# Optimization experiments

Measured on AMD Instinct MI355X. Metric: run time of the kernel, lower is better.

Reference implementation:

```python
import jax, jax.numpy as jnp
import numpy as np

TOP_K = 10
RANKING_WEIGHT = 0.3
UP_WEIGHT = 1.0
DOWN_WEIGHT = 0.5
NEG = 1e9  # finite stand-in for -inf so softmax/grads stay NaN-free


def setup_inputs() -> dict:
    key = jax.random.key(0)
    k1, k2, k3, k4 = jax.random.split(key, 4)
    B, N = 1024, 5000
    up_logits = jax.random.normal(k1, (B, N), jnp.float32)
    down_logits = jax.random.normal(k2, (B, N), jnp.float32)
    y_true = jax.random.normal(k3, (B, N), jnp.float32) * 0.05  # daily returns
    masks = jax.random.randint(k4, (B, N), 0, 2).astype(jnp.int32)
    return {"up_logits": up_logits, "down_logits": down_logits,
            "y_true": y_true, "masks": masks}


def _bce_with_logits(x, z):
    # softplus(x) - x*z  ==  -[z*log(sig(x)) + (1-z)*log(1-sig(x))]
    return jax.nn.softplus(x) - x * z


def reference(up_logits, down_logits, y_true, masks):
    maskb = masks > 0                                   # [B, N]
    maskf = maskb.astype(up_logits.dtype)
    num_valid = maskf.sum(-1)                           # [B]
    nv_safe = jnp.maximum(num_valid, 1.0)
    k = jnp.minimum(TOP_K, num_valid.astype(jnp.int32))  # [B] min(top_k, num)

    # Descending rank of y_true among valid entries (invalid pushed to bottom).
    y_desc = jnp.where(maskb, y_true, -NEG)
    rank_desc = jnp.argsort(jnp.argsort(-y_desc, axis=-1), axis=-1)  # [B, N]
    up_labels = (rank_desc < k[:, None]).astype(up_logits.dtype)

    # Ascending rank (biggest losers) for down path.
    y_asc = jnp.where(maskb, y_true, NEG)
    rank_asc = jnp.argsort(jnp.argsort(y_asc, axis=-1), axis=-1)
    down_labels = (rank_asc < k[:, None]).astype(down_logits.dtype)

    # Mean BCE over valid entries per row.
    up_loss = jnp.sum(_bce_with_logits(up_logits, up_labels) * maskf, -1) / nv_safe
    down_loss = jnp.sum(_bce_with_logits(down_logits, down_labels) * maskf, -1) / nv_safe

    # Listwise KL: softmax over valid entries; kl_div(log p, q, 'batchmean')
    # with 1D input of size num divides the sum by num.
    logp = jax.nn.log_softmax(jnp.where(maskb, up_logits, -NEG), axis=-1)
    logq = jax.nn.log_softmax(jnp.where(maskb, y_true, -NEG), axis=-1)
    q = jnp.exp(logq)
    kl = jnp.sum(jnp.where(maskb, q * (logq - logp), 0.0), -1) / nv_safe

    batch_loss = UP_WEIGHT * up_loss + DOWN_WEIGHT * down_loss + RANKING_WEIGHT * kl
    batch_loss = jnp.where(num_valid > 0, batch_loss, 0.0)  # skip empty rows
    return jnp.sum(batch_loss) / up_logits.shape[0]
```

## Files before the change

### kernel.cpp

```cpp
#include <hip/hip_runtime.h>
#include <math.h>

#define NCOLS 5000
#define NF4   1250
#define BLOCK 256
#define NWAVES (BLOCK / 64)
#define NITER 5
#define TOPKK 10
#define CAP 128

__device__ __forceinline__ unsigned mono_f32(float f) {
  unsigned u = __float_as_uint(f);
  return (u & 0x80000000u) ? ~u : (u | 0x80000000u);
}

__device__ __forceinline__ float wave_sum_f(float v) {
#pragma unroll
  for (int o = 1; o < 64; o <<= 1) v += __shfl_xor(v, o);
  return v;
}
__device__ __forceinline__ int wave_sum_i(int v) {
#pragma unroll
  for (int o = 1; o < 64; o <<= 1) v += __shfl_xor(v, o);
  return v;
}
__device__ __forceinline__ unsigned wave_max_u(unsigned v) {
#pragma unroll
  for (int o = 1; o < 64; o <<= 1) {
    unsigned w = __shfl_xor(v, o);
    v = w > v ? w : v;
  }
  return v;
}

extern "C" __global__ __launch_bounds__(BLOCK, 4)
void row_loss_kernel(const float* __restrict__ up, const float* __restrict__ down,
                     const float* __restrict__ yt, const int* __restrict__ masks,
                     float* __restrict__ out, float inv_nrows) {
  __shared__ float red_f[6][NWAVES];
  __shared__ int red_i[NWAVES];
  __shared__ unsigned t1w_t[NWAVES];
  __shared__ unsigned t1w_b[NWAVES];
  __shared__ unsigned keys_t[CAP];
  __shared__ int      col_t[CAP];
  __shared__ unsigned keys_b[CAP];
  __shared__ int      col_b[CAP];
  __shared__ int ct, cb;
  __shared__ float s_res[2];

  const int tid = threadIdx.x;
  const int lane = tid & 63;
  const int wv = tid >> 6;
  const int row = blockIdx.x;
  const long long b4 = (long long)row * NF4;
  const long long base = (long long)row * NCOLS;

  const float4* up4 = (const float4*)up + b4;
  const float4* dn4 = (const float4*)down + b4;
  const float4* yt4 = (const float4*)yt + b4;
  const int4*   mk4 = (const int4*)masks + b4;

  if (tid == 0) { ct = 0; cb = 0; }

  float4 y4[NITER], u4[NITER], d4[NITER];
  int4 m4[NITER];
#pragma unroll
  for (int j = 0; j < NITER; ++j) {
    const int f = j * BLOCK + tid;
    const int fc = f < NF4 ? f : NF4 - 1;
    y4[j] = yt4[fc];
    u4[j] = up4[fc];
    d4[j] = dn4[fc];
    m4[j] = mk4[fc];
  }

  unsigned km[NITER][4];
  int nv_l = 0;
  float sq = 0.f, sp = 0.f, seyy = 0.f, seyu = 0.f, aspu = 0.f, aspd = 0.f;
  unsigned tmax = 0u, tbmax = 0u;
#pragma unroll
  for (int j = 0; j < NITER; ++j) {
    const bool inb = (j * BLOCK + tid) < NF4;
    const float* yp = (const float*)&y4[j];
    const float* upp = (const float*)&u4[j];
    const float* dp = (const float*)&d4[j];
    const int* mp = (const int*)&m4[j];
#pragma unroll
    for (int c = 0; c < 4; ++c) {
      const bool valid = inb && (mp[c] > 0);
      const float y = yp[c], u = upp[c], d = dp[c];
      const unsigned kd = valid ? mono_f32(y) : 0u;
      const unsigned kb = valid ? ~kd : 0u;
      km[j][c] = kd;
      tmax = kd > tmax ? kd : tmax;
      tbmax = kb > tbmax ? kb : tbmax;
      if (valid) {
        nv_l++;
        const float ey = __expf(y);
        sq += ey;
        seyy += ey * y;
        seyu += ey * u;
        sp += __expf(u);
        aspu += fmaxf(u, 0.f) + __logf(1.f + __expf(-fabsf(u)));
        aspd += fmaxf(d, 0.f) + __logf(1.f + __expf(-fabsf(d)));
      }
    }
  }

  nv_l = wave_sum_i(nv_l);
  sq = wave_sum_f(sq);
  sp = wave_sum_f(sp);
  seyy = wave_sum_f(seyy);
  seyu = wave_sum_f(seyu);
  aspu = wave_sum_f(aspu);
  aspd = wave_sum_f(aspd);
  if (lane == 0) {
    red_i[wv] = nv_l;
    red_f[0][wv] = sq;  red_f[1][wv] = sp;
    red_f[2][wv] = seyy; red_f[3][wv] = seyu;
    red_f[4][wv] = aspu; red_f[5][wv] = aspd;
  }

  {
    unsigned v = tmax, t1 = 0u;
#pragma unroll 1
    for (int r = 0; r < TOPKK; ++r) {
      unsigned m = wave_max_u(v);
      if (v == m) v = 0u;
      t1 = m;
    }
    if (lane == 0) t1w_t[wv] = t1;
  }
  {
    unsigned v = tbmax, t1 = 0u;
#pragma unroll 1
    for (int r = 0; r < TOPKK; ++r) {
      unsigned m = wave_max_u(v);
      if (v == m) v = 0u;
      t1 = m;
    }
    if (lane == 0) t1w_b[wv] = t1;
  }
  __syncthreads();

  int nv = 0;
#pragma unroll
  for (int w = 0; w < NWAVES; ++w) nv += red_i[w];
  const int k = nv < TOPKK ? nv : TOPKK;

  unsigned t1 = 0u, t1b = 0u;
#pragma unroll
  for (int w = 0; w < NWAVES; ++w) {
    t1 = t1w_t[w] > t1 ? t1w_t[w] : t1;
    t1b = t1w_b[w] > t1b ? t1w_b[w] : t1b;
  }

#pragma unroll
  for (int j = 0; j < NITER; ++j) {
#pragma unroll
    for (int c = 0; c < 4; ++c) {
      const unsigned kd = km[j][c];
      if (kd != 0u) {
        const int col = ((j * BLOCK + tid) << 2) + c;
        if (kd >= t1) {
          int i = atomicAdd(&ct, 1);
          if (i < CAP) { keys_t[i] = kd; col_t[i] = col; }
        }
        const unsigned kb = ~kd;
        if (kb >= t1b) {
          int i = atomicAdd(&cb, 1);
          if (i < CAP) { keys_b[i] = kb; col_b[i] = col; }
        }
      }
    }
  }
  __syncthreads();

  if (wv == 0) {
    const int n = ct < CAP ? ct : CAP;
    unsigned k0 = (lane < n) ? keys_t[lane] : 0u;
    unsigned k1 = (64 + lane < n) ? keys_t[64 + lane] : 0u;
    unsigned w0 = k0, w1 = k1;
    unsigned thr = 0xFFFFFFFFu;
#pragma unroll 1
    for (int r = 0; r < k; ++r) {
      unsigned m = wave_max_u(w0 > w1 ? w0 : w1);
      if (w0 == m) w0 = 0u;
      else if (w1 == m) w1 = 0u;
      thr = m;
    }
    float su = 0.f;
    if (k0 >= thr && k0 != 0u) su += up[base + col_t[lane]];
    if (k1 >= thr && k1 != 0u) su += up[base + col_t[64 + lane]];
    su = wave_sum_f(su);
    if (lane == 0) s_res[0] = su;
  } else if (wv == 1) {
    const int n = cb < CAP ? cb : CAP;
    unsigned k0 = (lane < n) ? keys_b[lane] : 0u;
    unsigned k1 = (64 + lane < n) ? keys_b[64 + lane] : 0u;
    unsigned w0 = k0, w1 = k1;
    unsigned thr = 0xFFFFFFFFu;
#pragma unroll 1
    for (int r = 0; r < k; ++r) {
      unsigned m = wave_max_u(w0 > w1 ? w0 : w1);
      if (w0 == m) w0 = 0u;
      else if (w1 == m) w1 = 0u;
      thr = m;
    }
    float sd = 0.f;
    if (k0 >= thr && k0 != 0u) sd += down[base + col_b[lane]];
    if (k1 >= thr && k1 != 0u) sd += down[base + col_b[64 + lane]];
    sd = wave_sum_f(sd);
    if (lane == 0) s_res[1] = sd;
  }
  __syncthreads();

  if (tid == 0 && nv > 0) {
    float SQ = 0.f, SP = 0.f, SYY = 0.f, SYU = 0.f, ASU = 0.f, ASD = 0.f;
#pragma unroll
    for (int w = 0; w < NWAVES; ++w) {
      SQ += red_f[0][w]; SP += red_f[1][w];
      SYY += red_f[2][w]; SYU += red_f[3][w];
      ASU += red_f[4][w]; ASD += red_f[5][w];
    }
    const float SU = s_res[0];
    const float SD = s_res[1];
    const float kl = (SYY - SYU) / SQ - __logf(SQ) + __logf(SP);
    const float up_loss = ASU - SU;
    const float dn_loss = ASD - SD;
    const float loss = (up_loss + 0.5f * dn_loss + 0.3f * kl) / (float)nv;
    atomicAdd(out, loss * inv_nrows);
  }
}

extern "C" void kernel_launch(void* const* d_in, const int* in_sizes, int n_in,
                              void* d_out, int out_size, void* d_ws, size_t ws_size,
                              hipStream_t stream) {
  const float* up_logits   = (const float*)d_in[0];
  const float* down_logits = (const float*)d_in[1];
  const float* y_true      = (const float*)d_in[2];
  const int*   masks       = (const int*)d_in[3];

  const int nrows = in_sizes[0] / NCOLS;

  hipMemsetAsync(d_out, 0, sizeof(float) * (size_t)out_size, stream);
  row_loss_kernel<<<nrows, BLOCK, 0, stream>>>(up_logits, down_logits, y_true,
                                               masks, (float*)d_out,
                                               1.0f / (float)nrows);
}
```

Before: 124.2 us.

## Use 1024-thread blocks per row with per-thread top-2 candidate tracking

Each row is now processed by 1024 threads instead of 256. Loads and math are fused into a single pass that reads two float4 slots per thread. To keep candidate sets tight with more waves, each thread keeps its top two keys instead of only its max, and the candidate buffers grow to 512 entries with an 8-way per-lane selection loop. Softplus is simplified to log(1+exp(x)), which reuses exp(u); this risks overflow for very large logits. Occupancy bounds change as well, which may constrain registers.

```diff
diff --git a/kernel.cpp b/kernel.cpp
--- a/kernel.cpp
+++ b/kernel.cpp
@@ -3,11 +3,11 @@
 
 #define NCOLS 5000
 #define NF4   1250
-#define BLOCK 256
+#define BLOCK 1024
 #define NWAVES (BLOCK / 64)
-#define NITER 5
+#define NITER 2
 #define TOPKK 10
-#define CAP 128
+#define CAP 512
 
 __device__ __forceinline__ unsigned mono_f32(float f) {
   unsigned u = __float_as_uint(f);
@@ -33,7 +33,7 @@
   return v;
 }
 
-extern "C" __global__ __launch_bounds__(BLOCK, 4)
+extern "C" __global__ __launch_bounds__(BLOCK, 8)
 void row_loss_kernel(const float* __restrict__ up, const float* __restrict__ down,
                      const float* __restrict__ yt, const int* __restrict__ masks,
                      float* __restrict__ out, float inv_nrows) {
@@ -62,29 +62,23 @@
 
   if (tid == 0) { ct = 0; cb = 0; }
 
-  float4 y4[NITER], u4[NITER], d4[NITER];
-  int4 m4[NITER];
+  unsigned km[NITER][4];
+  int nv_l = 0;
+  float sq = 0.f, sp = 0.f, seyy = 0.f, seyu = 0.f, aspu = 0.f, aspd = 0.f;
+  unsigned a0 = 0u, a1 = 0u, bb0 = 0u, bb1 = 0u;
 #pragma unroll
   for (int j = 0; j < NITER; ++j) {
     const int f = j * BLOCK + tid;
     const int fc = f < NF4 ? f : NF4 - 1;
-    y4[j] = yt4[fc];
-    u4[j] = up4[fc];
-    d4[j] = dn4[fc];
-    m4[j] = mk4[fc];
-  }
-
-  unsigned km[NITER][4];
-  int nv_l = 0;
-  float sq = 0.f, sp = 0.f, seyy = 0.f, seyu = 0.f, aspu = 0.f, aspd = 0.f;
-  unsigned tmax = 0u, tbmax = 0u;
-#pragma unroll
-  for (int j = 0; j < NITER; ++j) {
-    const bool inb = (j * BLOCK + tid) < NF4;
-    const float* yp = (const float*)&y4[j];
-    const float* upp = (const float*)&u4[j];
-    const float* dp = (const float*)&d4[j];
-    const int* mp = (const int*)&m4[j];
+    const float4 y4 = yt4[fc];
+    const float4 u4 = up4[fc];
+    const float4 d4 = dn4[fc];
+    const int4   m4 = mk4[fc];
+    const bool inb = f < NF4;
+    const float* yp = (const float*)&y4;
+    const float* upp = (const float*)&u4;
+    const float* dp = (const float*)&d4;
+    const int* mp = (const int*)&m4;
 #pragma unroll
     for (int c = 0; c < 4; ++c) {
       const bool valid = inb && (mp[c] > 0);
@@ -92,17 +86,19 @@
       const unsigned kd = valid ? mono_f32(y) : 0u;
       const unsigned kb = valid ? ~kd : 0u;
       km[j][c] = kd;
-      tmax = kd > tmax ? kd : tmax;
-      tbmax = kb > tbmax ? kb : tbmax;
+      if (kd > a1) { if (kd > a0) { a1 = a0; a0 = kd; } else a1 = kd; }
+      if (kb > bb1) { if (kb > bb0) { bb1 = bb0; bb0 = kb; } else bb1 = kb; }
       if (valid) {
         nv_l++;
         const float ey = __expf(y);
+        const float eu = __expf(u);
+        const float ed = __expf(d);
         sq += ey;
         seyy += ey * y;
         seyu += ey * u;
-        sp += __expf(u);
-        aspu += fmaxf(u, 0.f) + __logf(1.f + __expf(-fabsf(u)));
-        aspd += fmaxf(d, 0.f) + __logf(1.f + __expf(-fabsf(d)));
+        sp += eu;
+        aspu += __logf(1.f + eu);
+        aspd += __logf(1.f + ed);
       }
     }
   }
@@ -122,21 +118,23 @@
   }
 
   {
-    unsigned v = tmax, t1 = 0u;
+    unsigned v0 = a0, v1 = a1, t1 = 0u;
 #pragma unroll 1
     for (int r = 0; r < TOPKK; ++r) {
-      unsigned m = wave_max_u(v);
-      if (v == m) v = 0u;
+      unsigned m = wave_max_u(v0 > v1 ? v0 : v1);
+      if (v0 == m) v0 = 0u;
+      else if (v1 == m) v1 = 0u;
       t1 = m;
     }
     if (lane == 0) t1w_t[wv] = t1;
   }
   {
-    unsigned v = tbmax, t1 = 0u;
+    unsigned v0 = bb0, v1 = bb1, t1 = 0u;
 #pragma unroll 1
     for (int r = 0; r < TOPKK; ++r) {
-      unsigned m = wave_max_u(v);
-      if (v == m) v = 0u;
+      unsigned m = wave_max_u(v0 > v1 ? v0 : v1);
+      if (v0 == m) v0 = 0u;
+      else if (v1 == m) v1 = 0u;
       t1 = m;
     }
     if (lane == 0) t1w_b[wv] = t1;
@@ -178,38 +176,78 @@
 
   if (wv == 0) {
     const int n = ct < CAP ? ct : CAP;
-    unsigned k0 = (lane < n) ? keys_t[lane] : 0u;
-    unsigned k1 = (64 + lane < n) ? keys_t[64 + lane] : 0u;
-    unsigned w0 = k0, w1 = k1;
+    unsigned kk[8];
+#pragma unroll
+    for (int i = 0; i < 8; ++i) {
+      const int idx = i * 64 + lane;
+      kk[i] = (idx < n) ? keys_t[idx] : 0u;
+    }
+    unsigned w0 = kk[0], w1 = kk[1], w2 = kk[2], w3 = kk[3];
+    unsigned w4 = kk[4], w5 = kk[5], w6 = kk[6], w7 = kk[7];
     unsigned thr = 0xFFFFFFFFu;
 #pragma unroll 1
     for (int r = 0; r < k; ++r) {
-      unsigned m = wave_max_u(w0 > w1 ? w0 : w1);
+      unsigned l0 = w0 > w1 ? w0 : w1;
+      unsigned l1 = w2 > w3 ? w2 : w3;
+      unsigned l2 = w4 > w5 ? w4 : w5;
+      unsigned l3 = w6 > w7 ? w6 : w7;
+      l0 = l0 > l1 ? l0 : l1;
+      l2 = l2 > l3 ? l2 : l3;
+      unsigned m = wave_max_u(l0 > l2 ? l0 : l2);
       if (w0 == m) w0 = 0u;
       else if (w1 == m) w1 = 0u;
+      else if (w2 == m) w2 = 0u;
+      else if (w3 == m) w3 = 0u;
+      else if (w4 == m) w4 = 0u;
+      else if (w5 == m) w5 = 0u;
+      else if (w6 == m) w6 = 0u;
+      else if (w7 == m) w7 = 0u;
       thr = m;
     }
     float su = 0.f;
-    if (k0 >= thr && k0 != 0u) su += up[base + col_t[lane]];
-    if (k1 >= thr && k1 != 0u) su += up[base + col_t[64 + lane]];
+#pragma unroll
+    for (int i = 0; i < 8; ++i) {
+      const int idx = i * 64 + lane;
+      if (kk[i] >= thr && kk[i] != 0u) su += up[base + col_t[idx]];
+    }
     su = wave_sum_f(su);
     if (lane == 0) s_res[0] = su;
   } else if (wv == 1) {
     const int n = cb < CAP ? cb : CAP;
-    unsigned k0 = (lane < n) ? keys_b[lane] : 0u;
-    unsigned k1 = (64 + lane < n) ? keys_b[64 + lane] : 0u;
-    unsigned w0 = k0, w1 = k1;
+    unsigned kk[8];
+#pragma unroll
+    for (int i = 0; i < 8; ++i) {
+      const int idx = i * 64 + lane;
+      kk[i] = (idx < n) ? keys_b[idx] : 0u;
+    }
+    unsigned w0 = kk[0], w1 = kk[1], w2 = kk[2], w3 = kk[3];
+    unsigned w4 = kk[4], w5 = kk[5], w6 = kk[6], w7 = kk[7];
     unsigned thr = 0xFFFFFFFFu;
 #pragma unroll 1
     for (int r = 0; r < k; ++r) {
-      unsigned m = wave_max_u(w0 > w1 ? w0 : w1);
+      unsigned l0 = w0 > w1 ? w0 : w1;
+      unsigned l1 = w2 > w3 ? w2 : w3;
+      unsigned l2 = w4 > w5 ? w4 : w5;
+      unsigned l3 = w6 > w7 ? w6 : w7;
+      l0 = l0 > l1 ? l0 : l1;
+      l2 = l2 > l3 ? l2 : l3;
+      unsigned m = wave_max_u(l0 > l2 ? l0 : l2);
       if (w0 == m) w0 = 0u;
       else if (w1 == m) w1 = 0u;
+      else if (w2 == m) w2 = 0u;
+      else if (w3 == m) w3 = 0u;
+      else if (w4 == m) w4 = 0u;
+      else if (w5 == m) w5 = 0u;
+      else if (w6 == m) w6 = 0u;
+      else if (w7 == m) w7 = 0u;
       thr = m;
     }
     float sd = 0.f;
-    if (k0 >= thr && k0 != 0u) sd += down[base + col_b[lane]];
-    if (k1 >= thr && k1 != 0u) sd += down[base + col_b[64 + lane]];
+#pragma unroll
+    for (int i = 0; i < 8; ++i) {
+      const int idx = i * 64 + lane;
+      if (kk[i] >= thr && kk[i] != 0u) sd += down[base + col_b[idx]];
+    }
     sd = wave_sum_f(sd);
     if (lane == 0) s_res[1] = sd;
   }
```

New measurement: 144.2 us. 1.16x slower.
